# Kernel optimization log

Measured on AMD Instinct MI355X. Metric: run time of the kernel, lower is better.

## Reference

```python
import jax, jax.numpy as jnp
import numpy as np

B, C, H, W = 4, 512, 64, 64
CA = C // 2  # attention hidden channels


def _conv1x1(x, w):
    # w: [O, I], x: [B, I, H, W]
    return jnp.einsum('oi,bihw->bohw', w, x)


def _conv3x3(x, w, b):
    y = jax.lax.conv_general_dilated(x, w, (1, 1), 'SAME',
                                     dimension_numbers=('NCHW', 'OIHW', 'NCHW'))
    return y + b[None, :, None, None]


def _scan_dir(x, w, b, axis, reverse):
    # IRNN recurrence along `axis`: prev = relu(prev * w + b + x_t), per-channel w,b.
    # The boundary position (first in scan order after un-flipping) stays zero,
    # matching the torch code which never writes it.
    xs = jnp.moveaxis(x, axis, 0)          # [L, B, C, other]
    if reverse:
        xs = xs[::-1]
    wb = w.reshape(1, -1, 1)
    bb = b.reshape(1, -1, 1)

    def step(prev, xt):
        new = jax.nn.relu(prev * wb + bb + xt)
        return new, new

    init = jax.nn.relu(xs[0])
    _, ys = jax.lax.scan(step, init, xs[1:])
    ys = jnp.concatenate([jnp.zeros_like(ys[:1]), ys], axis=0)
    if reverse:
        ys = ys[::-1]
    return jnp.moveaxis(ys, 0, axis)


def _irnn(x, wu, wr, wd, wl, bu, br, bd, bl):
    up = _scan_dir(x, wu, bu, 2, True)     # scans from bottom row upward
    right = _scan_dir(x, wr, br, 3, False)
    down = _scan_dir(x, wd, bd, 2, False)
    left = _scan_dir(x, wl, bl, 3, True)
    return up, right, down, left


def setup_inputs() -> dict:
    key = jax.random.key(0)
    ks = jax.random.split(key, 32)

    def n(k, shape, scale):
        return jax.random.normal(k, shape, jnp.float32) * scale

    inp = {
        'x': n(ks[0], (B, C, H, W), 1.0),
        # Attention: conv3x3(C->C/2)+b, conv3x3(C/2->C/2)+b, conv1x1(C/2->4)+b
        'a_w1': n(ks[1], (CA, C, 3, 3), (C * 9) ** -0.5),
        'a_b1': n(ks[2], (CA,), 0.02),
        'a_w2': n(ks[3], (CA, CA, 3, 3), (CA * 9) ** -0.5),
        'a_b2': n(ks[4], (CA,), 0.02),
        'a_w3': n(ks[5], (4, CA, 1, 1), CA ** -0.5),
        'a_b3': n(ks[6], (4,), 0.02),
        'cin_w': n(ks[7], (C, C), C ** -0.5),   # conv_in 1x1, bias=False
        'c2_w': n(ks[8], (C, 4 * C), (4 * C) ** -0.5),
        'c3_w': n(ks[9], (C, 4 * C), (4 * C) ** -0.5),
    }
    # IRNN per-channel recurrence weights (alpha=1.0 init) and biases
    i = 10
    for tag in ('i1', 'i2'):
        for d in ('u', 'r', 'd', 'l'):
            inp[f'{tag}_w{d}'] = jnp.ones((C,), jnp.float32)
            inp[f'{tag}_b{d}'] = n(ks[i], (C,), 0.05)
            i += 1
    return inp


def reference(x, a_w1, a_b1, a_w2, a_b2, a_w3, a_b3, cin_w,
              i1_wu, i1_bu, i1_wr, i1_br, i1_wd, i1_bd, i1_wl, i1_bl,
              c2_w,
              i2_wu, i2_bu, i2_wr, i2_br, i2_wd, i2_bd, i2_wl, i2_bl,
              c3_w):
    # Attention branch — computed but NEVER applied: the original torch code
    # uses out-of-place .mul() and discards the result (faithful reproduction).
    a = jax.nn.relu(_conv3x3(x, a_w1, a_b1))
    a = jax.nn.relu(_conv3x3(a, a_w2, a_b2))
    _weight = jax.nn.sigmoid(_conv1x1(a, a_w3[:, :, 0, 0]) + a_b3[None, :, None, None])

    out = _conv1x1(x, cin_w)
    u, r, d, l = _irnn(out, i1_wu, i1_wr, i1_wd, i1_wl, i1_bu, i1_br, i1_bd, i1_bl)
    out = jnp.concatenate([u, r, d, l], axis=1)   # [B, 4C, H, W]
    out = _conv1x1(out, c2_w)
    u, r, d, l = _irnn(out, i2_wu, i2_wr, i2_wd, i2_wl, i2_bu, i2_br, i2_bd, i2_bl)
    out = jnp.concatenate([u, r, d, l], axis=1)
    out = jax.nn.relu(_conv1x1(out, c3_w))
    return out
```

## Files before the change

kernel.cpp:

```cpp
#include <hip/hip_runtime.h>
#include <stdint.h>

#define NB 4
#define CB 512
#define HH 64
#define WW 64
#define HW 4096
#define C4 2048
#define PTOT (NB*HW)

typedef float  f32x4  __attribute__((ext_vector_type(4)));
typedef short  bf16x8 __attribute__((ext_vector_type(8)));

__device__ __forceinline__ float relu_f(float v){ return v > 0.f ? v : 0.f; }

__device__ __forceinline__ float bf2f(unsigned short u){
    union { uint32_t i; float f; } v; v.i = ((uint32_t)u) << 16; return v.f;
}
__device__ __forceinline__ unsigned short f2bf(float f){
    union { float f; uint32_t i; } v; v.f = f;
    uint32_t r = v.i + 0x7FFFu + ((v.i >> 16) & 1u);
    return (unsigned short)(r >> 16);
}

__device__ __forceinline__ void gload16(const void* g, void* l){
    __builtin_amdgcn_global_load_lds(
        (const __attribute__((address_space(1))) uint32_t*)g,
        (__attribute__((address_space(3))) uint32_t*)l, 16, 0, 0);
}

__global__ __launch_bounds__(256) void prep_fused(
    const float* __restrict__ x, unsigned short* __restrict__ xT,
    const float* __restrict__ a, unsigned short* __restrict__ oa,
    const float* __restrict__ b, unsigned short* __restrict__ ob,
    const float* __restrict__ c, unsigned short* __restrict__ oc)
{
    const int t = threadIdx.x;
    if (blockIdx.x >= 2048) {
        int i = (blockIdx.x - 2048) * 256 + t;
        const float* src; unsigned short* dst; int j;
        if (i < 65536)        { src = a; dst = oa; j = i; }
        else if (i < 327680)  { src = b; dst = ob; j = i - 65536; }
        else                  { src = c; dst = oc; j = i - 327680; }
        float4 v = ((const float4*)src)[j];
        ushort4 o;
        o.x = f2bf(v.x); o.y = f2bf(v.y); o.z = f2bf(v.z); o.w = f2bf(v.w);
        ((ushort4*)dst)[j] = o;
        return;
    }
    __shared__ unsigned short tile[64][72];
    const int tb = blockIdx.x;
    const int p0 = (tb & 63) * 64;
    const int c0 = ((tb >> 6) & 7) * 64;
    const int bb = tb >> 9;

    const int pl = (t & 15) * 4;
    const int cl = t >> 4;
    const float* src = x + ((size_t)bb * CB + c0) * HW + p0;
    #pragma unroll
    for (int r = 0; r < 4; r++) {
        int c2 = cl + r * 16;
        float4 v = *(const float4*)(src + (size_t)c2 * HW + pl);
        tile[pl + 0][c2] = f2bf(v.x);
        tile[pl + 1][c2] = f2bf(v.y);
        tile[pl + 2][c2] = f2bf(v.z);
        tile[pl + 3][c2] = f2bf(v.w);
    }
    __syncthreads();
    unsigned short* dst = xT + ((size_t)bb * HW + p0) * CB + c0;
    const int cl2 = (t & 15) * 4;
    const int pl2 = t >> 4;
    #pragma unroll
    for (int r = 0; r < 4; r++) {
        int p = pl2 + r * 16;
        ushort4 o = *(ushort4*)&tile[p][cl2];
        *(ushort4*)(dst + (size_t)p * CB + cl2) = o;
    }
}

template<int K, int OUTMODE>
__global__ __launch_bounds__(256) void gemm_cl(
    const unsigned short* __restrict__ A,
    const unsigned short* __restrict__ Bw,
    void* __restrict__ out)
{
    __shared__ __align__(16) char lds[65536];

    const int t    = threadIdx.x;
    const int lane = t & 63;
    const int wid  = t >> 6;
    const int p0   = blockIdx.x * 128;
    const int o0   = blockIdx.y * 128;

    const int l15 = lane & 15;
    const int l4  = lane >> 4;
    const int wp  = (wid & 1) * 64;
    const int wo  = (wid >> 1) * 64;
    const int rowA = wp + l15;
    const int rowB = wo + l15;
    const int swzA = (rowA & 7) << 4;
    const int swzB = (rowB & 7) << 4;

    f32x4 acc[4][4];
    #pragma unroll
    for (int m = 0; m < 4; m++)
        #pragma unroll
        for (int n = 0; n < 4; n++) acc[m][n] = (f32x4)0.f;

    const int srow  = t >> 3;
    const int scolb = (t & 7) * 16;

    auto STAGE = [&](int k0, char* base) {
        #pragma unroll
        for (int q = 0; q < 4; q++) {
            const int row = q * 32 + srow;
            const int kk  = k0 + ((scolb ^ ((row & 7) << 4)) >> 1);
            gload16(A  + (size_t)(p0 + row) * K + kk, base +         q * 4096 + wid * 1024);
            gload16(Bw + (size_t)(o0 + row) * K + kk, base + 16384 + q * 4096 + wid * 1024);
        }
    };
    auto COMPUTE = [&](const char* base) {
        const char* cA = base;
        const char* cB = base + 16384;
        #pragma unroll
        for (int kh = 0; kh < 2; kh++) {
            const int colb = kh * 64 + l4 * 16;
            bf16x8 a[4], b[4];
            #pragma unroll
            for (int m = 0; m < 4; m++)
                a[m] = *(const bf16x8*)(cA + (rowA + m * 16) * 128 + (colb ^ swzA));
            #pragma unroll
            for (int n = 0; n < 4; n++)
                b[n] = *(const bf16x8*)(cB + (rowB + n * 16) * 128 + (colb ^ swzB));
            __builtin_amdgcn_s_setprio(1);
            #pragma unroll
            for (int m = 0; m < 4; m++)
                #pragma unroll
                for (int n = 0; n < 4; n++)
                    acc[m][n] = __builtin_amdgcn_mfma_f32_16x16x32_bf16(
                                    a[m], b[n], acc[m][n], 0, 0, 0);
            __builtin_amdgcn_s_setprio(0);
        }
    };

    const int NT = K / 64;
    STAGE(0, lds);
    #pragma unroll 2
    for (int tt = 0; tt < NT - 1; ++tt) {
        char* cbase = lds + ((tt & 1) ? 32768 : 0);
        char* nbase = lds + ((tt & 1) ? 0 : 32768);
        STAGE((tt + 1) * 64, nbase);
        asm volatile("s_waitcnt vmcnt(8)" ::: "memory");
        __builtin_amdgcn_s_barrier();
        __builtin_amdgcn_sched_barrier(0);
        COMPUTE(cbase);
        __builtin_amdgcn_s_barrier();
    }
    asm volatile("s_waitcnt vmcnt(0)" ::: "memory");
    __builtin_amdgcn_s_barrier();
    __builtin_amdgcn_sched_barrier(0);
    COMPUTE(lds + (((NT - 1) & 1) ? 32768 : 0));

    if (OUTMODE == 0) {
        unsigned short* op = (unsigned short*)out;
        #pragma unroll
        for (int m = 0; m < 4; m++)
            #pragma unroll
            for (int r = 0; r < 4; r++) {
                const int p = p0 + wp + m * 16 + l4 * 4 + r;
                #pragma unroll
                for (int n = 0; n < 4; n++) {
                    const int o = wo + n * 16 + l15 + o0;
                    op[(size_t)p * CB + o] = f2bf(acc[m][n][r]);
                }
            }
    } else {
        __syncthreads();
        float (*tl)[132] = (float(*)[132])lds;
        const int bb   = p0 >> 12;
        const int phw0 = p0 & (HW - 1);
        #pragma unroll
        for (int half = 0; half < 2; half++) {
            if ((wid >> 1) == half) {
                #pragma unroll
                for (int n = 0; n < 4; n++)
                    #pragma unroll
                    for (int m = 0; m < 4; m++)
                        #pragma unroll
                        for (int r = 0; r < 4; r++)
                            tl[n * 16 + l15][wp + m * 16 + l4 * 4 + r] = acc[m][n][r];
            }
            __syncthreads();
            const int orow = t >> 2;
            const int pseg = (t & 3) * 32;
            float* dst = (float*)out +
                ((size_t)(bb * CB + o0 + half * 64 + orow)) * HW + phw0 + pseg;
            #pragma unroll
            for (int j = 0; j < 8; j++) {
                float4 v = *(float4*)&tl[orow][pseg + j * 4];
                v.x = relu_f(v.x); v.y = relu_f(v.y); v.z = relu_f(v.z); v.w = relu_f(v.w);
                *(float4*)(dst + j * 4) = v;
            }
            __syncthreads();
        }
    }
}

__global__ __launch_bounds__(256) void irnn_fused(
    const unsigned short* __restrict__ in, unsigned short* __restrict__ outc,
    const float* __restrict__ wu, const float* __restrict__ bu,
    const float* __restrict__ wr, const float* __restrict__ br,
    const float* __restrict__ wd, const float* __restrict__ bd,
    const float* __restrict__ wl, const float* __restrict__ bl)
{
    const int dir = blockIdx.y;
    const float* wv; const float* bv; int pstep, rev;
    if      (dir == 0) { wv = wu; bv = bu; pstep = 64; rev = 1; }
    else if (dir == 1) { wv = wr; bv = br; pstep = 1;  rev = 0; }
    else if (dir == 2) { wv = wd; bv = bd; pstep = 64; rev = 0; }
    else               { wv = wl; bv = bl; pstep = 1;  rev = 1; }
    const int dirOff = dir * 512;

    const int idx = blockIdx.x * 256 + threadIdx.x;
    const int c = idx & 511;
    const int f = (idx >> 9) & 63;
    const int b = idx >> 15;
    const int fbase = (pstep == 64) ? f : f * 64;

    const float wc = wv[c], bc = bv[c];
    const int t0 = rev ? 63 : 0;
    const int dp = rev ? -pstep : pstep;
    const int istep = dp * CB;
    const int ostep = dp * C4;

    const unsigned short* ip = in   + ((size_t)b * HW + fbase + (size_t)t0 * pstep) * CB + c;
    unsigned short*       op = outc + ((size_t)b * HW + fbase + (size_t)t0 * pstep) * C4 + dirOff + c;

    float s = relu_f(bf2f(ip[0]));
    op[0] = 0;

    unsigned short v0 = ip[1*istep], v1 = ip[2*istep], v2 = ip[3*istep], v3 = ip[4*istep],
                   v4 = ip[5*istep], v5 = ip[6*istep], v6 = ip[7*istep], v7 = ip[8*istep];

#define DO(kk, vv) { s = relu_f(fmaf(s, wc, bc + bf2f(vv))); op[(kk)*ostep] = f2bf(s); }
    for (int g = 0; g < 6; ++g) {
        const int k0 = 1 + 8 * g;
        DO(k0+0, v0); v0 = ip[(k0+ 8)*istep];
        DO(k0+1, v1); v1 = ip[(k0+ 9)*istep];
        DO(k0+2, v2); v2 = ip[(k0+10)*istep];
        DO(k0+3, v3); v3 = ip[(k0+11)*istep];
        DO(k0+4, v4); v4 = ip[(k0+12)*istep];
        DO(k0+5, v5); v5 = ip[(k0+13)*istep];
        DO(k0+6, v6); v6 = ip[(k0+14)*istep];
        DO(k0+7, v7); v7 = ip[(k0+15)*istep];
    }
    DO(49, v0); v0 = ip[57*istep];
    DO(50, v1); v1 = ip[58*istep];
    DO(51, v2); v2 = ip[59*istep];
    DO(52, v3); v3 = ip[60*istep];
    DO(53, v4); v4 = ip[61*istep];
    DO(54, v5); v5 = ip[62*istep];
    DO(55, v6); v6 = ip[63*istep];
    DO(56, v7);
    DO(57, v0); DO(58, v1); DO(59, v2); DO(60, v3);
    DO(61, v4); DO(62, v5); DO(63, v6);
#undef DO
}

extern "C" void kernel_launch(void* const* d_in, const int* in_sizes, int n_in,
                              void* d_out, int out_size, void* d_ws, size_t ws_size,
                              hipStream_t stream) {
    const float* x     = (const float*)d_in[0];
    const float* cin_w = (const float*)d_in[7];
    const float* c2_w  = (const float*)d_in[8];
    const float* c3_w  = (const float*)d_in[9];
    const float* i1_wu = (const float*)d_in[10];
    const float* i1_bu = (const float*)d_in[11];
    const float* i1_wr = (const float*)d_in[12];
    const float* i1_br = (const float*)d_in[13];
    const float* i1_wd = (const float*)d_in[14];
    const float* i1_bd = (const float*)d_in[15];
    const float* i1_wl = (const float*)d_in[16];
    const float* i1_bl = (const float*)d_in[17];
    const float* i2_wu = (const float*)d_in[18];
    const float* i2_bu = (const float*)d_in[19];
    const float* i2_wr = (const float*)d_in[20];
    const float* i2_br = (const float*)d_in[21];
    const float* i2_wd = (const float*)d_in[22];
    const float* i2_bd = (const float*)d_in[23];
    const float* i2_wl = (const float*)d_in[24];
    const float* i2_bl = (const float*)d_in[25];

    char* ws = (char*)d_ws;
    unsigned short* xT     = (unsigned short*)(ws);
    unsigned short* concat = (unsigned short*)(ws + (size_t)16 * 1024 * 1024);
    unsigned short* mid    = (unsigned short*)(ws + (size_t)80 * 1024 * 1024);
    unsigned short* wA     = (unsigned short*)(ws + (size_t)96 * 1024 * 1024);
    unsigned short* wB     = (unsigned short*)(wA + 512 * 512);
    unsigned short* wC     = (unsigned short*)(wB + 512 * 2048);

    prep_fused<<<4352, 256, 0, stream>>>(x, xT, cin_w, wA, c2_w, wB, c3_w, wC);

    dim3 ggrid(PTOT/128, 4);
    dim3 sgrid(512, 4);

    gemm_cl<512, 0><<<ggrid, 256, 0, stream>>>(xT, wA, mid);

    irnn_fused<<<sgrid, 256, 0, stream>>>(mid, concat,
        i1_wu, i1_bu, i1_wr, i1_br, i1_wd, i1_bd, i1_wl, i1_bl);

    gemm_cl<2048, 0><<<ggrid, 256, 0, stream>>>(concat, wB, mid);

    irnn_fused<<<sgrid, 256, 0, stream>>>(mid, concat,
        i2_wu, i2_bu, i2_wr, i2_br, i2_wd, i2_bd, i2_wl, i2_bl);

    gemm_cl<2048, 1><<<ggrid, 256, 0, stream>>>(concat, wC, d_out);
}
```

Baseline: 141.8 us.

## Triple-buffer A tiles and double-buffer B tiles in GEMM K-loop

Splits the staging of the GEMM K-loop into separate A and B loads. A tiles get a three-deep LDS ring (prefetched two tiles ahead) and B tiles stay double-buffered, with vmcnt waits adjusted to match. The aim is to hide more global-load latency behind MFMA compute. In exchange LDS per block rises from 64KB to 80KB, which may reduce occupancy, and the loop is no longer unrolled.

```diff
diff --git a/kernel.cpp b/kernel.cpp
--- a/kernel.cpp
+++ b/kernel.cpp
@@ -84,7 +84,7 @@
     const unsigned short* __restrict__ Bw,
     void* __restrict__ out)
 {
-    __shared__ __align__(16) char lds[65536];
+    __shared__ __align__(16) char lds[81920];
 
     const int t    = threadIdx.x;
     const int lane = t & 63;
@@ -110,18 +110,27 @@
     const int srow  = t >> 3;
     const int scolb = (t & 7) * 16;
 
-    auto STAGE = [&](int k0, char* base) {
+    auto A_STAGE = [&](int k0, int aoff) {
         #pragma unroll
         for (int q = 0; q < 4; q++) {
             const int row = q * 32 + srow;
             const int kk  = k0 + ((scolb ^ ((row & 7) << 4)) >> 1);
-            gload16(A  + (size_t)(p0 + row) * K + kk, base +         q * 4096 + wid * 1024);
-            gload16(Bw + (size_t)(o0 + row) * K + kk, base + 16384 + q * 4096 + wid * 1024);
+            gload16(A + (size_t)(p0 + row) * K + kk,
+                    lds + aoff + q * 4096 + wid * 1024);
         }
     };
-    auto COMPUTE = [&](const char* base) {
-        const char* cA = base;
-        const char* cB = base + 16384;
+    auto B_STAGE = [&](int k0, int boff) {
+        #pragma unroll
+        for (int q = 0; q < 4; q++) {
+            const int row = q * 32 + srow;
+            const int kk  = k0 + ((scolb ^ ((row & 7) << 4)) >> 1);
+            gload16(Bw + (size_t)(o0 + row) * K + kk,
+                    lds + boff + q * 4096 + wid * 1024);
+        }
+    };
+    auto COMPUTE = [&](int aoff, int boff) {
+        const char* cA = lds + aoff;
+        const char* cB = lds + boff;
         #pragma unroll
         for (int kh = 0; kh < 2; kh++) {
             const int colb = kh * 64 + l4 * 16;
@@ -144,22 +153,30 @@
     };
 
     const int NT = K / 64;
-    STAGE(0, lds);
-    #pragma unroll 2
-    for (int tt = 0; tt < NT - 1; ++tt) {
-        char* cbase = lds + ((tt & 1) ? 32768 : 0);
-        char* nbase = lds + ((tt & 1) ? 0 : 32768);
-        STAGE((tt + 1) * 64, nbase);
-        asm volatile("s_waitcnt vmcnt(8)" ::: "memory");
+    int aC = 0, aN = 16384, aF = 32768;
+
+    A_STAGE(0, aC);
+    B_STAGE(0, 49152);
+    A_STAGE(64, aN);
+
+    #pragma unroll 1
+    for (int tt = 0; tt < NT; ++tt) {
+        const int bC = 49152 + ((tt & 1) << 14);
+        const int bN = 49152 + (((tt + 1) & 1) << 14);
+        if (tt + 1 < NT) B_STAGE((tt + 1) * 64, bN);
+        if (tt + 2 < NT) A_STAGE((tt + 2) * 64, aF);
+
+        if (tt + 2 < NT)      asm volatile("s_waitcnt vmcnt(12)" ::: "memory");
+        else if (tt + 1 < NT) asm volatile("s_waitcnt vmcnt(8)"  ::: "memory");
+        else                  asm volatile("s_waitcnt vmcnt(0)"  ::: "memory");
         __builtin_amdgcn_s_barrier();
         __builtin_amdgcn_sched_barrier(0);
-        COMPUTE(cbase);
+
+        COMPUTE(aC, bC);
         __builtin_amdgcn_s_barrier();
-    }
-    asm volatile("s_waitcnt vmcnt(0)" ::: "memory");
-    __builtin_amdgcn_s_barrier();
-    __builtin_amdgcn_sched_barrier(0);
-    COMPUTE(lds + (((NT - 1) & 1) ? 32768 : 0));
+
+        const int tmp = aC; aC = aN; aN = aF; aF = tmp;
+    }
 
     if (OUTMODE == 0) {
         unsigned short* op = (unsigned short*)out;
```

Result: no change. 142.5 us (+0.5%).
